# Kernel optimization log

Measured on AMD Instinct MI355X. Metric: run time of the kernel, lower is better.

## Reference

```python
import jax, jax.numpy as jnp
import numpy as np


def _l2norm(x):
    # matches torch F.normalize(p=2, dim=-1) with eps clamp
    return x / jnp.clip(jnp.linalg.norm(x, axis=-1, keepdims=True), 1e-12)


def setup_inputs() -> dict:
    key = jax.random.key(0)
    k1, k2 = jax.random.split(key)
    I, J, S, H = 32, 32, 256, 768
    return {
        "query_embs": jax.random.normal(k1, (I, S, H), dtype=jnp.float32),
        "key_embs": jax.random.normal(k2, (J, S, H), dtype=jnp.float32),
        "q_mask": jnp.ones((I, S), dtype=jnp.float32),
        "k_mask": jnp.ones((J, S), dtype=jnp.float32),
        "alpha_raw": jnp.asarray(0.5, dtype=jnp.float32),  # learned scalar param
    }


def reference(query_embs, key_embs, q_mask, k_mask, alpha_raw):
    # eval path: gumbel_temp=None, use_max=False, do_distance=True, exp_decay=True
    S = query_embs.shape[1]
    pos = jnp.arange(S)
    distance = jnp.abs(pos[:, None] - pos[None, :]).astype(jnp.float32)  # [S, S]
    alpha = jax.nn.softplus(alpha_raw)

    qn = _l2norm(query_embs)  # [I, S, H]
    kn = _l2norm(key_embs)    # [J, T, H]

    # cross similarity [I, J, S, T] with exponential distance decay
    sim = jnp.einsum('ish,jth->ijst', qn, kn) * jnp.exp(-alpha * distance)

    # valid pair mask [I, J, S, T]
    valid = q_mask[:, None, :, None] * k_mask[None, :, None, :]
    masked = sim * valid - (1.0 - valid) * 1e9

    p = jax.nn.softmax(masked, axis=-1)             # softmax over key tokens t
    agg = jnp.einsum('ijst,jth->ijsh', p, kn)       # soft-aligned key embedding
    scores = jnp.einsum('ish,ijsh->ijs', qn, agg)   # per-query-token score
    scores = scores * q_mask[:, None, :]
    denom = jnp.clip(jnp.sum(q_mask, axis=-1, keepdims=True), 1.0)  # [I, 1]
    return jnp.sum(scores, axis=-1) / denom         # [I, J]
```

## Files before the change

kernel.cpp:

```cpp
#include <hip/hip_runtime.h>

#define I_DIM 32
#define J_DIM 32
#define S_DIM 256
#define H_DIM 768
#define KC    32
#define NCH   (H_DIM / KC)
#define TILE_B 32768
#define WSQ_BYTES ((size_t)I_DIM * NCH * TILE_B)
#define WSK_BYTES ((size_t)J_DIM * NCH * TILE_B)

typedef _Float16 f16x8 __attribute__((ext_vector_type(8)));
typedef float    f32x16 __attribute__((ext_vector_type(16)));

static __device__ __forceinline__ unsigned short f16bits(_Float16 h) {
    union { _Float16 f; unsigned short u; } cv; cv.f = h; return cv.u;
}

__global__ __launch_bounds__(256) void li_split_kernel(
    const float* __restrict__ qe, const float* __restrict__ ke,
    char* __restrict__ wsQ, char* __restrict__ wsK)
{
    const int lane = threadIdx.x & 63;
    const int w    = threadIdx.x >> 6;
    const int r    = blockIdx.x * 4 + w;
    const bool isQ = r < I_DIM * S_DIM;
    const int row  = isQ ? r : r - I_DIM * S_DIM;
    const float* base = (isQ ? qe : ke) + (size_t)row * H_DIM;

    float4 v[3];
    v[0] = *(const float4*)(base + 4 * lane);
    v[1] = *(const float4*)(base + 4 * lane + 256);
    v[2] = *(const float4*)(base + 4 * lane + 512);
    float ss = 0.0f;
    #pragma unroll
    for (int g = 0; g < 3; ++g)
        ss += v[g].x * v[g].x + v[g].y * v[g].y + v[g].z * v[g].z + v[g].w * v[g].w;
    #pragma unroll
    for (int m = 1; m < 64; m <<= 1) ss += __shfl_xor(ss, m, 64);
    const float inv = 1.0f / fmaxf(sqrtf(ss), 1e-12f);

    const int mi  = row >> 8;
    const int s   = row & 255;
    const int r7  = s & 7;
    char* wsb = (isQ ? wsQ : wsK) + (size_t)mi * NCH * TILE_B + s * 128;

    #pragma unroll
    for (int g = 0; g < 3; ++g) {
        const int k0 = 4 * lane + 256 * g;
        const int c  = k0 >> 5;
        const int kk = k0 & 31;
        float xn[4] = {v[g].x * inv, v[g].y * inv, v[g].z * inv, v[g].w * inv};
        unsigned short hb[4], lb[4];
        #pragma unroll
        for (int e = 0; e < 4; ++e) {
            _Float16 h  = (_Float16)xn[e];
            _Float16 lo = (_Float16)(xn[e] - (float)h);
            hb[e] = f16bits(h);
            lb[e] = f16bits(lo);
        }
        char* p = wsb + (size_t)c * TILE_B + (((kk >> 3) ^ r7) << 4) + (kk & 7) * 2;
        *(uint2*)(p)        = make_uint2(hb[0] | ((unsigned)hb[1] << 16), hb[2] | ((unsigned)hb[3] << 16));
        *(uint2*)((char*)((size_t)p ^ 64)) = make_uint2(lb[0] | ((unsigned)lb[1] << 16), lb[2] | ((unsigned)lb[3] << 16));
    }
}

__global__ __launch_bounds__(512, 2) void li_mfma_kernel(
    const char* __restrict__ wsQ, const char* __restrict__ wsK,
    const float* __restrict__ qm, const float* __restrict__ km,
    const float* __restrict__ alpha_raw, float* __restrict__ out)
{
    __shared__ __align__(16) char sQ[2][TILE_B];
    __shared__ __align__(16) char sK[2][TILE_B];
    __shared__ float kmsh[256], qmsh[256];
    __shared__ float pm[256][2], pL[256][2], pW[256][2];
    __shared__ float redA[512], redB[512];

    const int tid = threadIdx.x;
    const int wid = tid >> 6;
    const int l   = tid & 63;
    const int l31 = l & 31;
    const int hi  = l >> 5;
    const int wx  = wid & 1;
    const int wy  = wid >> 1;
    const int r7  = l31 & 7;

    const int bidx = blockIdx.x;
    const int x  = bidx & 7;
    const int r0 = bidx >> 3;
    const int j  = x * 4 + (r0 & 3);
    const int i  = r0 >> 2;

    if (tid < 256) {
        kmsh[tid] = km[j * 256 + tid];
        qmsh[tid] = qm[i * 256 + tid];
    }
    const float araw  = alpha_raw[0];
    const float alpha = (araw > 20.0f) ? araw : log1pf(expf(araw));
    const float nal   = -alpha;

    const char* qbase = wsQ + (size_t)i * NCH * TILE_B;
    const char* kbase = wsK + (size_t)j * NCH * TILE_B;

    f32x16 acc[2][4];
    #pragma unroll
    for (int mr = 0; mr < 2; ++mr)
        #pragma unroll
        for (int nt = 0; nt < 4; ++nt)
            #pragma unroll
            for (int z = 0; z < 16; ++z) acc[mr][nt][z] = 0.0f;

#define STAGE(buf, c)                                                                      \
    do {                                                                                   \
        const char* qt_ = qbase + (size_t)(c) * TILE_B + wid * 4096 + l * 16;              \
        const char* kt_ = kbase + (size_t)(c) * TILE_B + wid * 4096 + l * 16;              \
        char* dq_ = sQ[buf] + wid * 4096;                                                  \
        char* dk_ = sK[buf] + wid * 4096;                                                  \
        _Pragma("unroll")                                                                  \
        for (int u = 0; u < 4; ++u)                                                        \
            __builtin_amdgcn_global_load_lds(                                              \
                (const __attribute__((address_space(1))) void*)(qt_ + u * 1024),           \
                (__attribute__((address_space(3))) void*)(dq_ + u * 1024), 16, 0, 0);      \
        _Pragma("unroll")                                                                  \
        for (int u = 0; u < 4; ++u)                                                        \
            __builtin_amdgcn_global_load_lds(                                              \
                (const __attribute__((address_space(1))) void*)(kt_ + u * 1024),           \
                (__attribute__((address_space(3))) void*)(dk_ + u * 1024), 16, 0, 0);      \
    } while (0)

    STAGE(0, 0);
    asm volatile("s_waitcnt vmcnt(0)" ::: "memory");
    __builtin_amdgcn_sched_barrier(0);
    __builtin_amdgcn_s_barrier();
    __builtin_amdgcn_sched_barrier(0);

    for (int c = 0; c < NCH; ++c) {
        if (c + 1 < NCH) {
            STAGE((c + 1) & 1, c + 1);
            asm volatile("s_waitcnt vmcnt(8)" ::: "memory");
        } else {
            asm volatile("s_waitcnt vmcnt(0)" ::: "memory");
        }
        __builtin_amdgcn_sched_barrier(0);
        __builtin_amdgcn_s_barrier();
        __builtin_amdgcn_sched_barrier(0);

        const char* bQ = sQ[c & 1];
        const char* bK = sK[c & 1];
        #pragma unroll
        for (int ks = 0; ks < 2; ++ks) {
            const int soff = ((ks * 2 + hi) ^ r7) << 4;
            const int rA = wy * 64 + l31;
            const int rB = rA + 32;
            const f16x8 qhA = *(const f16x8*)(bQ + rA * 128 + soff);
            const f16x8 qlA = *(const f16x8*)(bQ + ((rA * 128 + soff) ^ 64));
            const f16x8 qhB = *(const f16x8*)(bQ + rB * 128 + soff);
            const f16x8 qlB = *(const f16x8*)(bQ + ((rB * 128 + soff) ^ 64));
            f16x8 kh[4], kl[4];
            #pragma unroll
            for (int nt = 0; nt < 4; ++nt) {
                const int rk = wx * 128 + nt * 32 + l31;
                kh[nt] = *(const f16x8*)(bK + rk * 128 + soff);
                kl[nt] = *(const f16x8*)(bK + ((rk * 128 + soff) ^ 64));
            }
            #pragma unroll
            for (int nt = 0; nt < 4; ++nt) {
                acc[0][nt] = __builtin_amdgcn_mfma_f32_32x32x16_f16(qhA, kh[nt], acc[0][nt], 0, 0, 0);
                acc[1][nt] = __builtin_amdgcn_mfma_f32_32x32x16_f16(qhB, kh[nt], acc[1][nt], 0, 0, 0);
            }
            #pragma unroll
            for (int nt = 0; nt < 4; ++nt) {
                acc[0][nt] = __builtin_amdgcn_mfma_f32_32x32x16_f16(qhA, kl[nt], acc[0][nt], 0, 0, 0);
                acc[1][nt] = __builtin_amdgcn_mfma_f32_32x32x16_f16(qhB, kl[nt], acc[1][nt], 0, 0, 0);
            }
            #pragma unroll
            for (int nt = 0; nt < 4; ++nt) {
                acc[0][nt] = __builtin_amdgcn_mfma_f32_32x32x16_f16(qlA, kh[nt], acc[0][nt], 0, 0, 0);
                acc[1][nt] = __builtin_amdgcn_mfma_f32_32x32x16_f16(qlB, kh[nt], acc[1][nt], 0, 0, 0);
            }
        }
        __builtin_amdgcn_sched_barrier(0);
        __builtin_amdgcn_s_barrier();
        __builtin_amdgcn_sched_barrier(0);
    }
#undef STAGE

    #pragma unroll
    for (int mrep = 0; mrep < 2; ++mrep) {
        #pragma unroll
        for (int reg = 0; reg < 16; ++reg) {
            const int srow = wy * 64 + mrep * 32 + hi * 4 + (reg & 3) + 8 * (reg >> 2);
            const float qms = qmsh[srow];
            float mv[4], cvv[4];
            float mloc = -3.0e38f;
            #pragma unroll
            for (int nt = 0; nt < 4; ++nt) {
                const int tcol = wx * 128 + nt * 32 + l31;
                const float cv = acc[mrep][nt][reg];
                int dd = srow - tcol; dd = dd < 0 ? -dd : dd;
                const float valid = qms * kmsh[tcol];
                const float m = cv * __expf(nal * (float)dd) * valid - (1.0f - valid) * 1e9f;
                mv[nt] = m; cvv[nt] = cv;
                mloc = fmaxf(mloc, m);
            }
            #pragma unroll
            for (int mm = 1; mm < 32; mm <<= 1)
                mloc = fmaxf(mloc, __shfl_xor(mloc, mm, 32));
            float L = 0.0f, W = 0.0f;
            #pragma unroll
            for (int nt = 0; nt < 4; ++nt) {
                const float e = __expf(mv[nt] - mloc);
                L += e;
                W += e * cvv[nt];
            }
            #pragma unroll
            for (int mm = 1; mm < 32; mm <<= 1) {
                L += __shfl_xor(L, mm, 32);
                W += __shfl_xor(W, mm, 32);
            }
            if (l31 == 0) {
                pm[srow][wx] = mloc;
                pL[srow][wx] = L;
                pW[srow][wx] = W;
            }
        }
    }
    __syncthreads();

    float contrib = 0.0f, qq = 0.0f;
    if (tid < 256) {
        const float m0 = pm[tid][0], m1 = pm[tid][1];
        const float M  = fmaxf(m0, m1);
        const float e0 = __expf(m0 - M), e1 = __expf(m1 - M);
        const float L  = pL[tid][0] * e0 + pL[tid][1] * e1;
        const float W  = pW[tid][0] * e0 + pW[tid][1] * e1;
        contrib = (W / L) * qmsh[tid];
        qq = qmsh[tid];
    }
    redA[tid] = contrib;
    redB[tid] = qq;
    __syncthreads();
    for (int off = 256; off > 0; off >>= 1) {
        if (tid < off) {
            redA[tid] += redA[tid + off];
            redB[tid] += redB[tid + off];
        }
        __syncthreads();
    }
    if (tid == 0) out[i * 32 + j] = redA[0] / fmaxf(redB[0], 1.0f);
}

extern "C" void kernel_launch(void* const* d_in, const int* in_sizes, int n_in,
                              void* d_out, int out_size, void* d_ws, size_t ws_size,
                              hipStream_t stream)
{
    const float* qe = (const float*)d_in[0];
    const float* ke = (const float*)d_in[1];
    const float* qm = (const float*)d_in[2];
    const float* km = (const float*)d_in[3];
    const float* al = (const float*)d_in[4];
    float* out = (float*)d_out;

    char* wsQ = (char*)d_ws;
    char* wsK = wsQ + WSQ_BYTES;

    hipLaunchKernelGGL(li_split_kernel, dim3((I_DIM + J_DIM) * S_DIM / 4), dim3(256),
                       0, stream, qe, ke, wsQ, wsK);
    hipLaunchKernelGGL(li_mfma_kernel, dim3(I_DIM * J_DIM), dim3(512), 0, stream,
                       wsQ, wsK, qm, km, al, out);
}
```

Before: 406.6 us.

## Split the 256x256 tile across 16 waves instead of 8

```diff
diff --git a/kernel.cpp b/kernel.cpp
--- a/kernel.cpp
+++ b/kernel.cpp
@@ -65,7 +65,7 @@
     }
 }
 
-__global__ __launch_bounds__(512, 2) void li_mfma_kernel(
+__global__ __launch_bounds__(1024, 4) void li_mfma_kernel(
     const char* __restrict__ wsQ, const char* __restrict__ wsK,
     const float* __restrict__ qm, const float* __restrict__ km,
     const float* __restrict__ alpha_raw, float* __restrict__ out)
@@ -73,16 +73,16 @@
     __shared__ __align__(16) char sQ[2][TILE_B];
     __shared__ __align__(16) char sK[2][TILE_B];
     __shared__ float kmsh[256], qmsh[256];
-    __shared__ float pm[256][2], pL[256][2], pW[256][2];
-    __shared__ float redA[512], redB[512];
+    __shared__ float pm[256][4], pL[256][4], pW[256][4];
+    __shared__ float redA[1024], redB[1024];
 
     const int tid = threadIdx.x;
     const int wid = tid >> 6;
     const int l   = tid & 63;
     const int l31 = l & 31;
     const int hi  = l >> 5;
-    const int wx  = wid & 1;
-    const int wy  = wid >> 1;
+    const int wx  = wid & 3;
+    const int wy  = wid >> 2;
     const int r7  = l31 & 7;
 
     const int bidx = blockIdx.x;
@@ -102,27 +102,27 @@
     const char* qbase = wsQ + (size_t)i * NCH * TILE_B;
     const char* kbase = wsK + (size_t)j * NCH * TILE_B;
 
-    f32x16 acc[2][4];
+    f32x16 acc[2][2];
     #pragma unroll
     for (int mr = 0; mr < 2; ++mr)
         #pragma unroll
-        for (int nt = 0; nt < 4; ++nt)
+        for (int nt = 0; nt < 2; ++nt)
             #pragma unroll
             for (int z = 0; z < 16; ++z) acc[mr][nt][z] = 0.0f;
 
 #define STAGE(buf, c)                                                                      \
     do {                                                                                   \
-        const char* qt_ = qbase + (size_t)(c) * TILE_B + wid * 4096 + l * 16;              \
-        const char* kt_ = kbase + (size_t)(c) * TILE_B + wid * 4096 + l * 16;              \
-        char* dq_ = sQ[buf] + wid * 4096;                                                  \
-        char* dk_ = sK[buf] + wid * 4096;                                                  \
+        const char* qt_ = qbase + (size_t)(c) * TILE_B + wid * 2048 + l * 16;              \
+        const char* kt_ = kbase + (size_t)(c) * TILE_B + wid * 2048 + l * 16;              \
+        char* dq_ = sQ[buf] + wid * 2048;                                                  \
+        char* dk_ = sK[buf] + wid * 2048;                                                  \
         _Pragma("unroll")                                                                  \
-        for (int u = 0; u < 4; ++u)                                                        \
+        for (int u = 0; u < 2; ++u)                                                        \
             __builtin_amdgcn_global_load_lds(                                              \
                 (const __attribute__((address_space(1))) void*)(qt_ + u * 1024),           \
                 (__attribute__((address_space(3))) void*)(dq_ + u * 1024), 16, 0, 0);      \
         _Pragma("unroll")                                                                  \
-        for (int u = 0; u < 4; ++u)                                                        \
+        for (int u = 0; u < 2; ++u)                                                        \
             __builtin_amdgcn_global_load_lds(                                              \
                 (const __attribute__((address_space(1))) void*)(kt_ + u * 1024),           \
                 (__attribute__((address_space(3))) void*)(dk_ + u * 1024), 16, 0, 0);      \
@@ -137,7 +137,7 @@
     for (int c = 0; c < NCH; ++c) {
         if (c + 1 < NCH) {
             STAGE((c + 1) & 1, c + 1);
-            asm volatile("s_waitcnt vmcnt(8)" ::: "memory");
+            asm volatile("s_waitcnt vmcnt(4)" ::: "memory");
         } else {
             asm volatile("s_waitcnt vmcnt(0)" ::: "memory");
         }
@@ -156,28 +156,27 @@
             const f16x8 qlA = *(const f16x8*)(bQ + ((rA * 128 + soff) ^ 64));
             const f16x8 qhB = *(const f16x8*)(bQ + rB * 128 + soff);
             const f16x8 qlB = *(const f16x8*)(bQ + ((rB * 128 + soff) ^ 64));
-            f16x8 kh[4], kl[4];
-            #pragma unroll
-            for (int nt = 0; nt < 4; ++nt) {
-                const int rk = wx * 128 + nt * 32 + l31;
-                kh[nt] = *(const f16x8*)(bK + rk * 128 + soff);
-                kl[nt] = *(const f16x8*)(bK + ((rk * 128 + soff) ^ 64));
-            }
-            #pragma unroll
-            for (int nt = 0; nt < 4; ++nt) {
-                acc[0][nt] = __builtin_amdgcn_mfma_f32_32x32x16_f16(qhA, kh[nt], acc[0][nt], 0, 0, 0);
-                acc[1][nt] = __builtin_amdgcn_mfma_f32_32x32x16_f16(qhB, kh[nt], acc[1][nt], 0, 0, 0);
-            }
-            #pragma unroll
-            for (int nt = 0; nt < 4; ++nt) {
-                acc[0][nt] = __builtin_amdgcn_mfma_f32_32x32x16_f16(qhA, kl[nt], acc[0][nt], 0, 0, 0);
-                acc[1][nt] = __builtin_amdgcn_mfma_f32_32x32x16_f16(qhB, kl[nt], acc[1][nt], 0, 0, 0);
-            }
-            #pragma unroll
-            for (int nt = 0; nt < 4; ++nt) {
-                acc[0][nt] = __builtin_amdgcn_mfma_f32_32x32x16_f16(qlA, kh[nt], acc[0][nt], 0, 0, 0);
-                acc[1][nt] = __builtin_amdgcn_mfma_f32_32x32x16_f16(qlB, kh[nt], acc[1][nt], 0, 0, 0);
-            }
+            const int c0 = wx * 64 + l31;
+            const int c1 = c0 + 32;
+            const f16x8 kh0 = *(const f16x8*)(bK + c0 * 128 + soff);
+            const f16x8 kl0 = *(const f16x8*)(bK + ((c0 * 128 + soff) ^ 64));
+            const f16x8 kh1 = *(const f16x8*)(bK + c1 * 128 + soff);
+            const f16x8 kl1 = *(const f16x8*)(bK + ((c1 * 128 + soff) ^ 64));
+
+            acc[0][0] = __builtin_amdgcn_mfma_f32_32x32x16_f16(qhA, kh0, acc[0][0], 0, 0, 0);
+            acc[0][1] = __builtin_amdgcn_mfma_f32_32x32x16_f16(qhA, kh1, acc[0][1], 0, 0, 0);
+            acc[1][0] = __builtin_amdgcn_mfma_f32_32x32x16_f16(qhB, kh0, acc[1][0], 0, 0, 0);
+            acc[1][1] = __builtin_amdgcn_mfma_f32_32x32x16_f16(qhB, kh1, acc[1][1], 0, 0, 0);
+
+            acc[0][0] = __builtin_amdgcn_mfma_f32_32x32x16_f16(qhA, kl0, acc[0][0], 0, 0, 0);
+            acc[0][1] = __builtin_amdgcn_mfma_f32_32x32x16_f16(qhA, kl1, acc[0][1], 0, 0, 0);
+            acc[1][0] = __builtin_amdgcn_mfma_f32_32x32x16_f16(qhB, kl0, acc[1][0], 0, 0, 0);
+            acc[1][1] = __builtin_amdgcn_mfma_f32_32x32x16_f16(qhB, kl1, acc[1][1], 0, 0, 0);
+
+            acc[0][0] = __builtin_amdgcn_mfma_f32_32x32x16_f16(qlA, kh0, acc[0][0], 0, 0, 0);
+            acc[0][1] = __builtin_amdgcn_mfma_f32_32x32x16_f16(qlA, kh1, acc[0][1], 0, 0, 0);
+            acc[1][0] = __builtin_amdgcn_mfma_f32_32x32x16_f16(qlB, kh0, acc[1][0], 0, 0, 0);
+            acc[1][1] = __builtin_amdgcn_mfma_f32_32x32x16_f16(qlB, kh1, acc[1][1], 0, 0, 0);
         }
         __builtin_amdgcn_sched_barrier(0);
         __builtin_amdgcn_s_barrier();
@@ -186,17 +185,17 @@
 #undef STAGE
 
     #pragma unroll
-    for (int mrep = 0; mrep < 2; ++mrep) {
-        #pragma unroll
-        for (int reg = 0; reg < 16; ++reg) {
-            const int srow = wy * 64 + mrep * 32 + hi * 4 + (reg & 3) + 8 * (reg >> 2);
+    for (int mr = 0; mr < 2; ++mr) {
+        #pragma unroll
+        for (int z = 0; z < 16; ++z) {
+            const int srow = wy * 64 + mr * 32 + hi * 4 + (z & 3) + 8 * (z >> 2);
             const float qms = qmsh[srow];
-            float mv[4], cvv[4];
+            float mv[2], cvv[2];
             float mloc = -3.0e38f;
             #pragma unroll
-            for (int nt = 0; nt < 4; ++nt) {
-                const int tcol = wx * 128 + nt * 32 + l31;
-                const float cv = acc[mrep][nt][reg];
+            for (int nt = 0; nt < 2; ++nt) {
+                const int tcol = wx * 64 + nt * 32 + l31;
+                const float cv = acc[mr][nt][z];
                 int dd = srow - tcol; dd = dd < 0 ? -dd : dd;
                 const float valid = qms * kmsh[tcol];
                 const float m = cv * __expf(nal * (float)dd) * valid - (1.0f - valid) * 1e9f;
@@ -208,7 +207,7 @@
                 mloc = fmaxf(mloc, __shfl_xor(mloc, mm, 32));
             float L = 0.0f, W = 0.0f;
             #pragma unroll
-            for (int nt = 0; nt < 4; ++nt) {
+            for (int nt = 0; nt < 2; ++nt) {
                 const float e = __expf(mv[nt] - mloc);
                 L += e;
                 W += e * cvv[nt];
@@ -229,18 +228,21 @@
 
     float contrib = 0.0f, qq = 0.0f;
     if (tid < 256) {
-        const float m0 = pm[tid][0], m1 = pm[tid][1];
-        const float M  = fmaxf(m0, m1);
-        const float e0 = __expf(m0 - M), e1 = __expf(m1 - M);
-        const float L  = pL[tid][0] * e0 + pL[tid][1] * e1;
-        const float W  = pW[tid][0] * e0 + pW[tid][1] * e1;
+        float M = fmaxf(fmaxf(pm[tid][0], pm[tid][1]), fmaxf(pm[tid][2], pm[tid][3]));
+        float L = 0.0f, W = 0.0f;
+        #pragma unroll
+        for (int q = 0; q < 4; ++q) {
+            const float e = __expf(pm[tid][q] - M);
+            L += pL[tid][q] * e;
+            W += pW[tid][q] * e;
+        }
         contrib = (W / L) * qmsh[tid];
         qq = qmsh[tid];
     }
     redA[tid] = contrib;
     redB[tid] = qq;
     __syncthreads();
-    for (int off = 256; off > 0; off >>= 1) {
+    for (int off = 512; off > 0; off >>= 1) {
         if (tid < off) {
             redA[tid] += redA[tid + off];
             redB[tid] += redB[tid + off];
@@ -266,6 +268,6 @@
 
     hipLaunchKernelGGL(li_split_kernel, dim3((I_DIM + J_DIM) * S_DIM / 4), dim3(256),
                        0, stream, qe, ke, wsQ, wsK);
-    hipLaunchKernelGGL(li_mfma_kernel, dim3(I_DIM * J_DIM), dim3(512), 0, stream,
+    hipLaunchKernelGGL(li_mfma_kernel, dim3(I_DIM * J_DIM), dim3(1024), 0, stream,
                        wsQ, wsK, qm, km, al, out);
 }
```

Measured after the change: 441.1 us. +8.5%, slower.
